# Optimization experiments

Measured on AMD Instinct MI355X. Metric: run time of the kernel, lower is better.

## Reference

```python
import jax, jax.numpy as jnp
import numpy as np

B, N, D, OUT, ED = 8, 256, 128, 128, 1

def setup_inputs() -> dict:
    key = jax.random.key(0)
    ks = jax.random.split(key, 10)
    in2 = 2 * D + ED  # 257
    s = lambda f: 1.0 / np.sqrt(f)
    return {
        "h": jax.random.normal(ks[0], (B, N, D), dtype=jnp.float32),
        "adj": jax.random.randint(ks[1], (B, N, N), 0, 2, dtype=jnp.int32),
        "dist_matrix": jax.random.uniform(ks[2], (B, N, N), dtype=jnp.float32),
        "Wm1": jax.random.uniform(ks[3], (in2, OUT), minval=-s(in2), maxval=s(in2)),
        "bm1": jnp.zeros((OUT,), jnp.float32),
        "Wm2": jax.random.uniform(ks[4], (OUT, OUT), minval=-s(OUT), maxval=s(OUT)),
        "bm2": jnp.zeros((OUT,), jnp.float32),
        "Wa": jax.random.uniform(ks[5], (in2, 1), minval=-s(in2), maxval=s(in2)),
        "ba": jnp.zeros((1,), jnp.float32),
        "Wu": jax.random.uniform(ks[6], (D + OUT, OUT), minval=-s(D + OUT), maxval=s(D + OUT)),
        "bu": jnp.zeros((OUT,), jnp.float32),
    }

def reference(h, adj, dist_matrix, Wm1, bm1, Wm2, bm2, Wa, ba, Wu, bu):
    # h: (B,N,D); adj,dist: (B,N,N)
    Bb, Nn, Dd = h.shape
    h_i = jnp.broadcast_to(h[:, :, None, :], (Bb, Nn, Nn, Dd))
    h_j = jnp.broadcast_to(h[:, None, :, :], (Bb, Nn, Nn, Dd))
    d_ij = dist_matrix[..., None]
    msg_input = jnp.concatenate([h_i, h_j, d_ij], axis=-1)  # (B,N,N,2D+1)
    # message MLP: Linear -> ReLU -> Linear
    msg = jax.nn.relu(msg_input @ Wm1 + bm1) @ Wm2 + bm2    # (B,N,N,OUT)
    # attention MLP: Linear -> LeakyReLU(0.2)
    attn = jax.nn.leaky_relu(msg_input @ Wa + ba, 0.2)      # (B,N,N,1)
    mask = adj[..., None].astype(msg.dtype)                  # (B,N,N,1)
    attn = jnp.where(mask == 0, jnp.asarray(-1e9, attn.dtype), attn)
    attn = jax.nn.softmax(attn, axis=2)                      # softmax over j
    agg = jnp.sum(attn * msg * mask, axis=2)                 # (B,N,OUT)
    h_new = jax.nn.relu(jnp.concatenate([h, agg], axis=-1) @ Wu + bu)
    return h_new
```

## Files before the change

kernel.cpp:

```cpp
#include <hip/hip_runtime.h>

#define BB 8
#define NN 256
#define DD 128
#define OC 128

__global__ __launch_bounds__(128) void precompute_kernel(
    const float* __restrict__ h, const float* __restrict__ Wm1,
    const float* __restrict__ Wa,
    float* __restrict__ preA, float* __restrict__ preB,
    float* __restrict__ ai, float* __restrict__ aj)
{
    const int row = blockIdx.x;
    const int k   = threadIdx.x;

    __shared__ float hrow[DD];
    hrow[k] = h[row * DD + k];
    __syncthreads();

    float accA = 0.f, accB = 0.f;
    #pragma unroll 8
    for (int d = 0; d < DD; ++d) {
        const float hv = hrow[d];
        accA = fmaf(hv, Wm1[d * OC + k], accA);
        accB = fmaf(hv, Wm1[(DD + d) * OC + k], accB);
    }
    preA[row * OC + k] = accA;
    preB[row * OC + k] = accB;

    float vi = hrow[k] * Wa[k];
    float vj = hrow[k] * Wa[DD + k];
    #pragma unroll
    for (int off = 32; off > 0; off >>= 1) {
        vi += __shfl_down(vi, off, 64);
        vj += __shfl_down(vj, off, 64);
    }
    __shared__ float red[4];
    if ((k & 63) == 0) { red[(k >> 6) * 2] = vi; red[(k >> 6) * 2 + 1] = vj; }
    __syncthreads();
    if (k == 0) { ai[row] = red[0] + red[2]; aj[row] = red[1] + red[3]; }
}

__global__ __launch_bounds__(256) void gnn_main_kernel(
    const float* __restrict__ h, const int* __restrict__ adj,
    const float* __restrict__ dist,
    const float* __restrict__ Wm1, const float* __restrict__ bm1,
    const float* __restrict__ Wm2, const float* __restrict__ bm2,
    const float* __restrict__ Wa,  const float* __restrict__ ba,
    const float* __restrict__ Wu,  const float* __restrict__ bu,
    const float* __restrict__ preA, const float* __restrict__ preB,
    const float* __restrict__ aiArr, const float* __restrict__ ajArr,
    float* __restrict__ out)
{
    const int row  = blockIdx.x;
    const int b    = row >> 8;
    const int tid  = threadIdx.x;
    const int k    = tid & (OC - 1);
    const int half = tid >> 7;

    __shared__ float w_sh[NN];
    __shared__ float d_sh[NN];
    __shared__ float red_sh[256];
    __shared__ float t_sh[OC];
    __shared__ float agg_sh[OC];
    __shared__ float preA_sh[OC];
    __shared__ float hrow_sh[DD];
    __shared__ float wsum_sh;

    const int   j  = tid;
    const float dv = dist[row * NN + j];
    const int   mk = adj[row * NN + j];
    d_sh[j] = dv;

    float logit = aiArr[row] + ajArr[b * NN + j] + dv * Wa[2 * DD] + ba[0];
    logit = (logit >= 0.f) ? logit : 0.2f * logit;
    if (mk == 0) logit = -1e9f;

    red_sh[tid] = logit;
    __syncthreads();
    #pragma unroll
    for (int s = 128; s > 0; s >>= 1) {
        if (tid < s) red_sh[tid] = fmaxf(red_sh[tid], red_sh[tid + s]);
        __syncthreads();
    }
    const float mx = red_sh[0];
    __syncthreads();

    const float e = __expf(logit - mx);
    red_sh[tid] = e;
    __syncthreads();
    #pragma unroll
    for (int s = 128; s > 0; s >>= 1) {
        if (tid < s) red_sh[tid] += red_sh[tid + s];
        __syncthreads();
    }
    const float esum = red_sh[0];
    const float w = mk ? (e / esum) : 0.f;
    w_sh[j] = w;
    __syncthreads();

    red_sh[tid] = w;
    if (tid < OC)   preA_sh[tid]        = preA[row * OC + tid];
    if (tid >= 128) hrow_sh[tid - 128]  = h[row * DD + (tid - 128)];
    __syncthreads();
    #pragma unroll
    for (int s = 128; s > 0; s >>= 1) {
        if (tid < s) red_sh[tid] += red_sh[tid + s];
        __syncthreads();
    }
    if (tid == 0) wsum_sh = red_sh[0];
    __syncthreads();

    const float wm1d = Wm1[2 * DD * OC + k];
    const float bm1k = bm1[k];
    const float pa   = preA_sh[k];
    const float* __restrict__ pB = preB + b * NN * OC;

    float acc = 0.f;
    const int j0 = half * 128;
    for (int jj = j0; jj < j0 + 128; ++jj) {
        const float wj = w_sh[jj];
        if (wj != 0.f) {
            float val = fmaf(d_sh[jj], wm1d, pa + pB[jj * OC + k]) + bm1k;
            acc = fmaf(wj, fmaxf(val, 0.f), acc);
        }
    }
    red_sh[tid] = acc;
    __syncthreads();
    if (tid < OC) t_sh[tid] = red_sh[tid] + red_sh[tid + 128];
    __syncthreads();

    float aggacc = 0.f;
    const int m0 = half * 64;
    #pragma unroll 4
    for (int m = m0; m < m0 + 64; ++m)
        aggacc = fmaf(t_sh[m], Wm2[m * OC + k], aggacc);
    red_sh[tid] = aggacc;
    __syncthreads();
    if (tid < OC) agg_sh[tid] = red_sh[tid] + red_sh[tid + 128] + bm2[tid] * wsum_sh;
    __syncthreads();

    float outacc = 0.f;
    if (half == 0) {
        #pragma unroll 4
        for (int d2 = 0; d2 < DD; ++d2)
            outacc = fmaf(hrow_sh[d2], Wu[d2 * OC + k], outacc);
    } else {
        #pragma unroll 4
        for (int m = 0; m < OC; ++m)
            outacc = fmaf(agg_sh[m], Wu[(DD + m) * OC + k], outacc);
    }
    red_sh[tid] = outacc;
    __syncthreads();
    if (tid < OC)
        out[row * OC + tid] = fmaxf(red_sh[tid] + red_sh[tid + 128] + bu[tid], 0.f);
}

extern "C" void kernel_launch(void* const* d_in, const int* in_sizes, int n_in,
                              void* d_out, int out_size, void* d_ws, size_t ws_size,
                              hipStream_t stream) {
    const float* h    = (const float*)d_in[0];
    const int*   adj  = (const int*)  d_in[1];
    const float* dist = (const float*)d_in[2];
    const float* Wm1  = (const float*)d_in[3];
    const float* bm1  = (const float*)d_in[4];
    const float* Wm2  = (const float*)d_in[5];
    const float* bm2  = (const float*)d_in[6];
    const float* Wa   = (const float*)d_in[7];
    const float* ba   = (const float*)d_in[8];
    const float* Wu   = (const float*)d_in[9];
    const float* bu   = (const float*)d_in[10];
    float* out = (float*)d_out;

    float* preA = (float*)d_ws;
    float* preB = preA + BB * NN * OC;
    float* ai   = preB + BB * NN * OC;
    float* aj   = ai + BB * NN;

    precompute_kernel<<<BB * NN, 128, 0, stream>>>(h, Wm1, Wa, preA, preB, ai, aj);
    gnn_main_kernel<<<BB * NN, 256, 0, stream>>>(h, adj, dist,
                                                 Wm1, bm1, Wm2, bm2, Wa, ba, Wu, bu,
                                                 preA, preB, ai, aj, out);
}
```

Measured before the change: 125.8 us.

## Split GNN into three kernels with tiled GEMMs and compacted neighbor loop

Replaces the two-kernel design with three kernels. A multi-row precompute GEMM now also produces the h·Wu term. The main kernel uses wave-shuffle softmax reductions and ballot-compacts the active neighbors into shared memory, then loops only over them with float2 loads. A separate batched kernel does the Wm2 and Wu GEMMs over 8 rows with tiled shared weights. The aim is to cut the per-row redundant weight reads and the barrier-heavy tree reductions, at the cost of an extra launch and an intermediate matrix in global memory.

```diff
diff --git a/kernel.cpp b/kernel.cpp
--- a/kernel.cpp
+++ b/kernel.cpp
@@ -1,159 +1,234 @@
 #include <hip/hip_runtime.h>
 
-#define BB 8
 #define NN 256
 #define DD 128
 #define OC 128
 
-__global__ __launch_bounds__(128) void precompute_kernel(
+__global__ __launch_bounds__(256) void k1_pre(
     const float* __restrict__ h, const float* __restrict__ Wm1,
-    const float* __restrict__ Wa,
-    float* __restrict__ preA, float* __restrict__ preB,
-    float* __restrict__ ai, float* __restrict__ aj)
+    const float* __restrict__ Wa, const float* __restrict__ bm1,
+    const float* __restrict__ Wu, const float* __restrict__ ba,
+    float* __restrict__ pre, float* __restrict__ aiv, float* __restrict__ ajv)
 {
-    const int row = blockIdx.x;
-    const int k   = threadIdx.x;
-
-    __shared__ float hrow[DD];
-    hrow[k] = h[row * DD + k];
-    __syncthreads();
-
-    float accA = 0.f, accB = 0.f;
-    #pragma unroll 8
-    for (int d = 0; d < DD; ++d) {
-        const float hv = hrow[d];
-        accA = fmaf(hv, Wm1[d * OC + k], accA);
-        accB = fmaf(hv, Wm1[(DD + d) * OC + k], accB);
-    }
-    preA[row * OC + k] = accA;
-    preB[row * OC + k] = accB;
-
-    float vi = hrow[k] * Wa[k];
-    float vj = hrow[k] * Wa[DD + k];
-    #pragma unroll
-    for (int off = 32; off > 0; off >>= 1) {
-        vi += __shfl_down(vi, off, 64);
-        vj += __shfl_down(vj, off, 64);
-    }
-    __shared__ float red[4];
-    if ((k & 63) == 0) { red[(k >> 6) * 2] = vi; red[(k >> 6) * 2 + 1] = vj; }
-    __syncthreads();
-    if (k == 0) { ai[row] = red[0] + red[2]; aj[row] = red[1] + red[3]; }
-}
-
-__global__ __launch_bounds__(256) void gnn_main_kernel(
-    const float* __restrict__ h, const int* __restrict__ adj,
-    const float* __restrict__ dist,
-    const float* __restrict__ Wm1, const float* __restrict__ bm1,
-    const float* __restrict__ Wm2, const float* __restrict__ bm2,
-    const float* __restrict__ Wa,  const float* __restrict__ ba,
-    const float* __restrict__ Wu,  const float* __restrict__ bu,
-    const float* __restrict__ preA, const float* __restrict__ preB,
-    const float* __restrict__ aiArr, const float* __restrict__ ajArr,
-    float* __restrict__ out)
+    const int tid  = threadIdx.x;
+    const int row0 = blockIdx.x * 4;
+    const int r    = tid >> 6;
+    const int g    = tid & 63;
+
+    __shared__ float h_sh[4][128];
+    __shared__ float w_sh[16][384];
+
+    const float2* h2    = (const float2*)h;
+    const float2* Wm1_2 = (const float2*)Wm1;
+    const float2* Wu_2  = (const float2*)Wu;
+    const float2* Wa2   = (const float2*)Wa;
+
+    ((float2*)h_sh)[tid] = h2[row0 * 64 + tid];
+    __syncthreads();
+
+    {
+        float2 hv = ((const float2*)h_sh[r])[g];
+        float2 wt = Wa2[g], wb = Wa2[64 + g];
+        float vi = hv.x * wt.x + hv.y * wt.y;
+        float vj = hv.x * wb.x + hv.y * wb.y;
+        #pragma unroll
+        for (int o = 1; o < 64; o <<= 1) {
+            vi += __shfl_xor(vi, o, 64);
+            vj += __shfl_xor(vj, o, 64);
+        }
+        if (g == 0) { aiv[row0 + r] = vi + ba[0]; ajv[row0 + r] = vj; }
+    }
+
+    float2 a0{0.f,0.f}, a1{0.f,0.f}, a2{0.f,0.f};
+    for (int c = 0; c < 8; ++c) {
+        const int d0 = c * 16;
+        __syncthreads();
+        #pragma unroll
+        for (int v = 0; v < 12; ++v) {
+            int idx = tid + 256 * v;
+            int dd = idx / 192, cc = idx % 192;
+            int srow = d0 + dd;
+            float2 val;
+            if (cc < 64)       val = Wm1_2[srow * 64 + cc];
+            else if (cc < 128) val = Wm1_2[(128 + srow) * 64 + (cc - 64)];
+            else               val = Wu_2[srow * 64 + (cc - 128)];
+            ((float2*)w_sh[dd])[cc] = val;
+        }
+        __syncthreads();
+        #pragma unroll
+        for (int dd = 0; dd < 16; ++dd) {
+            const float hb = h_sh[r][d0 + dd];
+            const float2* wr2 = (const float2*)w_sh[dd];
+            float2 w0 = wr2[g], w1 = wr2[64 + g], w2v = wr2[128 + g];
+            a0.x = fmaf(hb, w0.x,  a0.x); a0.y = fmaf(hb, w0.y,  a0.y);
+            a1.x = fmaf(hb, w1.x,  a1.x); a1.y = fmaf(hb, w1.y,  a1.y);
+            a2.x = fmaf(hb, w2v.x, a2.x); a2.y = fmaf(hb, w2v.y, a2.y);
+        }
+    }
+    const float2 bb = ((const float2*)bm1)[g];
+    a0.x += bb.x; a0.y += bb.y;
+    float2* pre2 = (float2*)pre;
+    const int rbase = (row0 + r) * 192;
+    pre2[rbase + g]       = a0;
+    pre2[rbase + 64 + g]  = a1;
+    pre2[rbase + 128 + g] = a2;
+}
+
+__global__ __launch_bounds__(256) void k2_main(
+    const int* __restrict__ adj, const float* __restrict__ dist,
+    const float* __restrict__ Wm1, const float* __restrict__ Wa,
+    const float* __restrict__ pre,
+    const float* __restrict__ aiv, const float* __restrict__ ajv,
+    float* __restrict__ tmat, float* __restrict__ sflag)
 {
     const int row  = blockIdx.x;
     const int b    = row >> 8;
     const int tid  = threadIdx.x;
-    const int k    = tid & (OC - 1);
-    const int half = tid >> 7;
-
-    __shared__ float w_sh[NN];
-    __shared__ float d_sh[NN];
-    __shared__ float red_sh[256];
-    __shared__ float t_sh[OC];
-    __shared__ float agg_sh[OC];
-    __shared__ float preA_sh[OC];
-    __shared__ float hrow_sh[DD];
-    __shared__ float wsum_sh;
+    const int lane = tid & 63;
+    const int wid  = tid >> 6;
+
+    __shared__ float4 cwd[4][64];
+    __shared__ float  mx_sh[4], sm_sh[4];
+    __shared__ float2 tred[4][64];
 
     const int   j  = tid;
     const float dv = dist[row * NN + j];
     const int   mk = adj[row * NN + j];
-    d_sh[j] = dv;
-
-    float logit = aiArr[row] + ajArr[b * NN + j] + dv * Wa[2 * DD] + ba[0];
+
+    float logit = aiv[row] + ajv[b * NN + j] + dv * Wa[2 * DD];
     logit = (logit >= 0.f) ? logit : 0.2f * logit;
-    if (mk == 0) logit = -1e9f;
-
-    red_sh[tid] = logit;
-    __syncthreads();
+    const float lmask = mk ? logit : -1e9f;
+
+    float m = lmask;
     #pragma unroll
-    for (int s = 128; s > 0; s >>= 1) {
-        if (tid < s) red_sh[tid] = fmaxf(red_sh[tid], red_sh[tid + s]);
-        __syncthreads();
-    }
-    const float mx = red_sh[0];
-    __syncthreads();
-
-    const float e = __expf(logit - mx);
-    red_sh[tid] = e;
-    __syncthreads();
+    for (int o = 1; o < 64; o <<= 1) m = fmaxf(m, __shfl_xor(m, o, 64));
+    if (lane == 0) mx_sh[wid] = m;
+    __syncthreads();
+    const float mx = fmaxf(fmaxf(mx_sh[0], mx_sh[1]), fmaxf(mx_sh[2], mx_sh[3]));
+
+    float em = mk ? __expf(logit - mx) : 0.f;
+    float s = em;
     #pragma unroll
-    for (int s = 128; s > 0; s >>= 1) {
-        if (tid < s) red_sh[tid] += red_sh[tid + s];
-        __syncthreads();
-    }
-    const float esum = red_sh[0];
-    const float w = mk ? (e / esum) : 0.f;
-    w_sh[j] = w;
-    __syncthreads();
-
-    red_sh[tid] = w;
-    if (tid < OC)   preA_sh[tid]        = preA[row * OC + tid];
-    if (tid >= 128) hrow_sh[tid - 128]  = h[row * DD + (tid - 128)];
-    __syncthreads();
-    #pragma unroll
-    for (int s = 128; s > 0; s >>= 1) {
-        if (tid < s) red_sh[tid] += red_sh[tid + s];
-        __syncthreads();
-    }
-    if (tid == 0) wsum_sh = red_sh[0];
-    __syncthreads();
-
-    const float wm1d = Wm1[2 * DD * OC + k];
-    const float bm1k = bm1[k];
-    const float pa   = preA_sh[k];
-    const float* __restrict__ pB = preB + b * NN * OC;
-
-    float acc = 0.f;
-    const int j0 = half * 128;
-    for (int jj = j0; jj < j0 + 128; ++jj) {
-        const float wj = w_sh[jj];
-        if (wj != 0.f) {
-            float val = fmaf(d_sh[jj], wm1d, pa + pB[jj * OC + k]) + bm1k;
-            acc = fmaf(wj, fmaxf(val, 0.f), acc);
-        }
-    }
-    red_sh[tid] = acc;
-    __syncthreads();
-    if (tid < OC) t_sh[tid] = red_sh[tid] + red_sh[tid + 128];
-    __syncthreads();
-
-    float aggacc = 0.f;
-    const int m0 = half * 64;
-    #pragma unroll 4
-    for (int m = m0; m < m0 + 64; ++m)
-        aggacc = fmaf(t_sh[m], Wm2[m * OC + k], aggacc);
-    red_sh[tid] = aggacc;
-    __syncthreads();
-    if (tid < OC) agg_sh[tid] = red_sh[tid] + red_sh[tid + 128] + bm2[tid] * wsum_sh;
-    __syncthreads();
-
-    float outacc = 0.f;
-    if (half == 0) {
-        #pragma unroll 4
-        for (int d2 = 0; d2 < DD; ++d2)
-            outacc = fmaf(hrow_sh[d2], Wu[d2 * OC + k], outacc);
-    } else {
-        #pragma unroll 4
-        for (int m = 0; m < OC; ++m)
-            outacc = fmaf(agg_sh[m], Wu[(DD + m) * OC + k], outacc);
-    }
-    red_sh[tid] = outacc;
-    __syncthreads();
-    if (tid < OC)
-        out[row * OC + tid] = fmaxf(red_sh[tid] + red_sh[tid + 128] + bu[tid], 0.f);
+    for (int o = 1; o < 64; o <<= 1) s += __shfl_xor(s, o, 64);
+    if (lane == 0) sm_sh[wid] = s;
+    __syncthreads();
+    const float esum = sm_sh[0] + sm_sh[1] + sm_sh[2] + sm_sh[3];
+    const float inv  = (esum > 0.f) ? (1.0f / esum) : 0.f;
+    const float w    = em * inv;
+
+    const unsigned long long act = __ballot(w != 0.f);
+    const int pos = __popcll(act & ((1ull << lane) - 1ull));
+    const int cnt = __popcll(act);
+    if (w != 0.f)
+        cwd[wid][pos] = make_float4(w, dv, __int_as_float(j * 192), 0.f);
+    __syncthreads();
+
+    const float2* pre2 = (const float2*)pre;
+    const float2  pa   = pre2[row * 192 + lane];
+    const float2  wd1  = ((const float2*)Wm1)[(2 * DD * OC) / 2 + lane];
+    const float2* pB   = pre2 + (size_t)b * NN * 192 + 64;
+
+    float2 acc{0.f, 0.f};
+    for (int i = 0; i < cnt; ++i) {
+        float4 c = cwd[wid][i];
+        int off = __float_as_int(c.z);
+        float2 pb = pB[off + lane];
+        float vx = fmaf(c.y, wd1.x, pa.x + pb.x);
+        float vy = fmaf(c.y, wd1.y, pa.y + pb.y);
+        acc.x = fmaf(c.x, fmaxf(vx, 0.f), acc.x);
+        acc.y = fmaf(c.x, fmaxf(vy, 0.f), acc.y);
+    }
+    tred[wid][lane] = acc;
+    __syncthreads();
+    if (tid < 64) {
+        float2 t0 = tred[0][tid], t1 = tred[1][tid];
+        float2 t2v = tred[2][tid], t3 = tred[3][tid];
+        float2 tt{t0.x + t1.x + t2v.x + t3.x, t0.y + t1.y + t2v.y + t3.y};
+        ((float2*)tmat)[row * 64 + tid] = tt;
+    }
+    if (tid == 0) sflag[row] = (esum > 0.f) ? 1.f : 0.f;
+}
+
+__global__ __launch_bounds__(256) void k3_out(
+    const float* __restrict__ tmat, const float* __restrict__ sflag,
+    const float* __restrict__ pre,
+    const float* __restrict__ Wm2, const float* __restrict__ bm2,
+    const float* __restrict__ Wu,  const float* __restrict__ bu,
+    float* __restrict__ out)
+{
+    const int tid  = threadIdx.x;
+    const int row0 = blockIdx.x * 8;
+    const int r    = tid >> 5;
+    const int g    = tid & 31;
+
+    __shared__ float t_sh[8][128];
+    __shared__ float agg_sh[8][128];
+    __shared__ float w_sh[16][128];
+    __shared__ float sf_sh[8];
+
+    const float2* t2 = (const float2*)tmat;
+    ((float2*)t_sh)[tid]       = t2[row0 * 64 + tid];
+    ((float2*)t_sh)[tid + 256] = t2[row0 * 64 + tid + 256];
+    if (tid < 8) sf_sh[tid] = sflag[row0 + tid];
+
+    const float2* Wm2_2 = (const float2*)Wm2;
+    const float2* Wu_2  = (const float2*)Wu;
+
+    float2 a0{0.f,0.f}, a1{0.f,0.f};
+    for (int c = 0; c < 8; ++c) {
+        const int d0 = c * 16;
+        __syncthreads();
+        #pragma unroll
+        for (int v = 0; v < 4; ++v) {
+            int idx = tid + 256 * v;
+            int dd = idx >> 6, cc = idx & 63;
+            ((float2*)w_sh)[idx] = Wm2_2[(d0 + dd) * 64 + cc];
+        }
+        __syncthreads();
+        #pragma unroll
+        for (int dd = 0; dd < 16; ++dd) {
+            const float tb = t_sh[r][d0 + dd];
+            const float2* wr2 = (const float2*)w_sh[dd];
+            float2 w0 = wr2[g], w1 = wr2[32 + g];
+            a0.x = fmaf(tb, w0.x, a0.x); a0.y = fmaf(tb, w0.y, a0.y);
+            a1.x = fmaf(tb, w1.x, a1.x); a1.y = fmaf(tb, w1.y, a1.y);
+        }
+    }
+    const float sf = sf_sh[r];
+    const float2 b0 = ((const float2*)bm2)[g], b1 = ((const float2*)bm2)[32 + g];
+    ((float2*)agg_sh[r])[g]      = make_float2(fmaf(b0.x, sf, a0.x), fmaf(b0.y, sf, a0.y));
+    ((float2*)agg_sh[r])[32 + g] = make_float2(fmaf(b1.x, sf, a1.x), fmaf(b1.y, sf, a1.y));
+
+    a0 = make_float2(0.f, 0.f); a1 = make_float2(0.f, 0.f);
+    for (int c = 0; c < 8; ++c) {
+        const int d0 = c * 16;
+        __syncthreads();
+        #pragma unroll
+        for (int v = 0; v < 4; ++v) {
+            int idx = tid + 256 * v;
+            int dd = idx >> 6, cc = idx & 63;
+            ((float2*)w_sh)[idx] = Wu_2[(128 + d0 + dd) * 64 + cc];
+        }
+        __syncthreads();
+        #pragma unroll
+        for (int dd = 0; dd < 16; ++dd) {
+            const float ab = agg_sh[r][d0 + dd];
+            const float2* wr2 = (const float2*)w_sh[dd];
+            float2 w0 = wr2[g], w1 = wr2[32 + g];
+            a0.x = fmaf(ab, w0.x, a0.x); a0.y = fmaf(ab, w0.y, a0.y);
+            a1.x = fmaf(ab, w1.x, a1.x); a1.y = fmaf(ab, w1.y, a1.y);
+        }
+    }
+
+    const float2* pre2 = (const float2*)pre;
+    const int prow = (row0 + r) * 192 + 128;
+    float2 hu0 = pre2[prow + g], hu1 = pre2[prow + 32 + g];
+    float2 c0 = ((const float2*)bu)[g], c1 = ((const float2*)bu)[32 + g];
+    float2 o0{fmaxf(a0.x + hu0.x + c0.x, 0.f), fmaxf(a0.y + hu0.y + c0.y, 0.f)};
+    float2 o1{fmaxf(a1.x + hu1.x + c1.x, 0.f), fmaxf(a1.y + hu1.y + c1.y, 0.f)};
+    float2* out2 = (float2*)out;
+    out2[(row0 + r) * 64 + g]      = o0;
+    out2[(row0 + r) * 64 + 32 + g] = o1;
 }
 
 extern "C" void kernel_launch(void* const* d_in, const int* in_sizes, int n_in,
@@ -172,13 +247,13 @@
     const float* bu   = (const float*)d_in[10];
     float* out = (float*)d_out;
 
-    float* preA = (float*)d_ws;
-    float* preB = preA + BB * NN * OC;
-    float* ai   = preB + BB * NN * OC;
-    float* aj   = ai + BB * NN;
-
-    precompute_kernel<<<BB * NN, 128, 0, stream>>>(h, Wm1, Wa, preA, preB, ai, aj);
-    gnn_main_kernel<<<BB * NN, 256, 0, stream>>>(h, adj, dist,
-                                                 Wm1, bm1, Wm2, bm2, Wa, ba, Wu, bu,
-                                                 preA, preB, ai, aj, out);
-}
+    float* pre   = (float*)d_ws;
+    float* aiv   = pre + 2048 * 384;
+    float* ajv   = aiv + 2048;
+    float* tmat  = ajv + 2048;
+    float* sfl   = tmat + 2048 * 128;
+
+    k1_pre <<<512, 256, 0, stream>>>(h, Wm1, Wa, bm1, Wu, ba, pre, aiv, ajv);
+    k2_main<<<2048, 256, 0, stream>>>(adj, dist, Wm1, Wa, pre, aiv, ajv, tmat, sfl);
+    k3_out <<<256, 256, 0, stream>>>(tmat, sfl, pre, Wm2, bm2, Wu, bu, out);
+}
```

Result: slower. 133.6 us (+6.2%).

## Split GNN into three wave-per-row kernels with compacted neighbor lists

Applied to the files above, without the earlier changes.

Replaces the two-kernel design with three kernels that each map one 64-lane wave to a row. The precompute kernel now also folds in the h·Wu half of the update and the bm1 bias, using readlane broadcasts and float2 loads. The main kernel does the softmax with wave shuffles instead of shared-memory tree reductions, compacts the non-zero neighbours via ballot/popcount, and loops only over those. The Wm2 and Wu matmuls move into a separate output kernel. This cuts barriers and predicated loop iterations, at the cost of an extra launch and a round trip of intermediate results through global memory.

```diff
diff --git a/kernel.cpp b/kernel.cpp
--- a/kernel.cpp
+++ b/kernel.cpp
@@ -1,159 +1,215 @@
 #include <hip/hip_runtime.h>
 
-#define BB 8
 #define NN 256
 #define DD 128
 #define OC 128
 
-__global__ __launch_bounds__(128) void precompute_kernel(
+__device__ __forceinline__ float bcastf(float x, int lane) {
+    return __int_as_float(__builtin_amdgcn_readlane(__float_as_int(x), lane));
+}
+
+__global__ __launch_bounds__(256) void k1_pre(
     const float* __restrict__ h, const float* __restrict__ Wm1,
-    const float* __restrict__ Wa,
-    float* __restrict__ preA, float* __restrict__ preB,
-    float* __restrict__ ai, float* __restrict__ aj)
+    const float* __restrict__ Wa, const float* __restrict__ bm1,
+    const float* __restrict__ Wu, const float* __restrict__ ba,
+    float* __restrict__ pre, float* __restrict__ aiv, float* __restrict__ ajv)
 {
-    const int row = blockIdx.x;
-    const int k   = threadIdx.x;
-
-    __shared__ float hrow[DD];
-    hrow[k] = h[row * DD + k];
-    __syncthreads();
-
-    float accA = 0.f, accB = 0.f;
-    #pragma unroll 8
-    for (int d = 0; d < DD; ++d) {
-        const float hv = hrow[d];
-        accA = fmaf(hv, Wm1[d * OC + k], accA);
-        accB = fmaf(hv, Wm1[(DD + d) * OC + k], accB);
-    }
-    preA[row * OC + k] = accA;
-    preB[row * OC + k] = accB;
-
-    float vi = hrow[k] * Wa[k];
-    float vj = hrow[k] * Wa[DD + k];
+    const int tid = threadIdx.x;
+    const int l   = tid & 63;
+    const int w   = tid >> 6;
+    const int row = blockIdx.x * 4 + w;
+
+    const float2* h2v   = (const float2*)h;
+    const float2* Wm1_2 = (const float2*)Wm1;
+    const float2* Wu_2  = (const float2*)Wu;
+    const float2* Wa2   = (const float2*)Wa;
+
+    const float2 hl = h2v[row * 64 + l];
+
+    {
+        const float2 wt = Wa2[l], wb = Wa2[64 + l];
+        float vi = hl.x * wt.x + hl.y * wt.y;
+        float vj = hl.x * wb.x + hl.y * wb.y;
+        #pragma unroll
+        for (int o = 1; o < 64; o <<= 1) {
+            vi += __shfl_xor(vi, o, 64);
+            vj += __shfl_xor(vj, o, 64);
+        }
+        if (l == 0) { aiv[row] = vi + ba[0]; ajv[row] = vj; }
+    }
+
+    float2 c0{0.f,0.f}, c1{0.f,0.f}, c2{0.f,0.f};
+    #pragma unroll 4
+    for (int m = 0; m < 64; ++m) {
+        const float hx = bcastf(hl.x, m);
+        const float hy = bcastf(hl.y, m);
+        const int d0 = 2 * m, d1 = 2 * m + 1;
+        const float2 a00 = Wm1_2[d0 * 64 + l],        a01 = Wm1_2[d1 * 64 + l];
+        const float2 b00 = Wm1_2[(DD + d0) * 64 + l], b01 = Wm1_2[(DD + d1) * 64 + l];
+        const float2 u00 = Wu_2[d0 * 64 + l],         u01 = Wu_2[d1 * 64 + l];
+        c0.x = fmaf(hx, a00.x, fmaf(hy, a01.x, c0.x));
+        c0.y = fmaf(hx, a00.y, fmaf(hy, a01.y, c0.y));
+        c1.x = fmaf(hx, b00.x, fmaf(hy, b01.x, c1.x));
+        c1.y = fmaf(hx, b00.y, fmaf(hy, b01.y, c1.y));
+        c2.x = fmaf(hx, u00.x, fmaf(hy, u01.x, c2.x));
+        c2.y = fmaf(hx, u00.y, fmaf(hy, u01.y, c2.y));
+    }
+    const float2 bb = ((const float2*)bm1)[l];
+    c0.x += bb.x; c0.y += bb.y;
+
+    float2* pre2 = (float2*)pre;
+    const int rb = row * 192;
+    pre2[rb + l]       = c0;
+    pre2[rb + 64 + l]  = c1;
+    pre2[rb + 128 + l] = c2;
+}
+
+__global__ __launch_bounds__(256) void k2_main(
+    const int* __restrict__ adj, const float* __restrict__ dist,
+    const float* __restrict__ Wm1, const float* __restrict__ Wa,
+    const float* __restrict__ pre,
+    const float* __restrict__ aiv, const float* __restrict__ ajv,
+    float* __restrict__ tmat, float* __restrict__ sflag)
+{
+    const int tid  = threadIdx.x;
+    const int l    = tid & 63;
+    const int wid  = tid >> 6;
+    const int r    = wid >> 1;
+    const int half = wid & 1;
+    const int row  = blockIdx.x * 2 + r;
+    const int b    = row >> 8;
+
+    __shared__ float  mx_sh[4], sm_sh[4];
+    __shared__ float4 cw[4][128];
+    __shared__ float2 accb[2][64];
+
+    const int   jb  = half * 128;
+    const int2  mk2 = ((const int2*)  (adj  + row * NN))[half * 64 + l];
+    const float2 dv2 = ((const float2*)(dist + row * NN))[half * 64 + l];
+    const float2 aj2 = ((const float2*)(ajv  + b   * NN))[half * 64 + l];
+    const float ai = aiv[row];
+    const float dc = Wa[2 * DD];
+
+    float l0 = ai + aj2.x + dv2.x * dc;
+    float l1 = ai + aj2.y + dv2.y * dc;
+    l0 = (l0 >= 0.f) ? l0 : 0.2f * l0;
+    l1 = (l1 >= 0.f) ? l1 : 0.2f * l1;
+    const float l0m = mk2.x ? l0 : -1e9f;
+    const float l1m = mk2.y ? l1 : -1e9f;
+
+    float m = fmaxf(l0m, l1m);
     #pragma unroll
-    for (int off = 32; off > 0; off >>= 1) {
-        vi += __shfl_down(vi, off, 64);
-        vj += __shfl_down(vj, off, 64);
-    }
-    __shared__ float red[4];
-    if ((k & 63) == 0) { red[(k >> 6) * 2] = vi; red[(k >> 6) * 2 + 1] = vj; }
-    __syncthreads();
-    if (k == 0) { ai[row] = red[0] + red[2]; aj[row] = red[1] + red[3]; }
-}
-
-__global__ __launch_bounds__(256) void gnn_main_kernel(
-    const float* __restrict__ h, const int* __restrict__ adj,
-    const float* __restrict__ dist,
-    const float* __restrict__ Wm1, const float* __restrict__ bm1,
+    for (int o = 1; o < 64; o <<= 1) m = fmaxf(m, __shfl_xor(m, o, 64));
+    if (l == 0) mx_sh[wid] = m;
+    __syncthreads();
+    const float mx = fmaxf(mx_sh[r * 2], mx_sh[r * 2 + 1]);
+
+    const float e0 = mk2.x ? __expf(l0 - mx) : 0.f;
+    const float e1 = mk2.y ? __expf(l1 - mx) : 0.f;
+    float s = e0 + e1;
+    #pragma unroll
+    for (int o = 1; o < 64; o <<= 1) s += __shfl_xor(s, o, 64);
+    if (l == 0) sm_sh[wid] = s;
+    __syncthreads();
+    const float esum = sm_sh[r * 2] + sm_sh[r * 2 + 1];
+    const float inv  = (esum > 0.f) ? (1.0f / esum) : 0.f;
+    const float w0 = e0 * inv, w1 = e1 * inv;
+
+    const unsigned long long below = (1ull << l) - 1ull;
+    const unsigned long long m0 = __ballot(w0 != 0.f);
+    const unsigned long long m1 = __ballot(w1 != 0.f);
+    const int c0n = __popcll(m0);
+    const int cnt = c0n + __popcll(m1);
+    const int j0 = jb + 2 * l;
+    if (w0 != 0.f)
+        cw[wid][__popcll(m0 & below)]       = make_float4(w0, dv2.x, __int_as_float(j0 * 192), 0.f);
+    if (w1 != 0.f)
+        cw[wid][c0n + __popcll(m1 & below)] = make_float4(w1, dv2.y, __int_as_float((j0 + 1) * 192), 0.f);
+    __syncthreads();
+    const float4 g0 = cw[wid][l];
+    const float4 g1 = cw[wid][64 + l];
+
+    const float2* pre2 = (const float2*)pre;
+    const float2  pa   = pre2[row * 192 + l];
+    const float2  wd1  = ((const float2*)Wm1)[(2 * DD * OC) / 2 + l];
+    const float2* pBb  = pre2 + (size_t)b * NN * 192 + 64;
+
+    float2 acc{0.f, 0.f};
+    const int n0 = cnt < 64 ? cnt : 64;
+    for (int p = 0; p < n0; ++p) {
+        const float wp  = bcastf(g0.x, p);
+        const float dp  = bcastf(g0.y, p);
+        const int   jof = __builtin_amdgcn_readlane(__float_as_int(g0.z), p);
+        const float2 pb = pBb[jof + l];
+        const float vx = fmaf(dp, wd1.x, pa.x + pb.x);
+        const float vy = fmaf(dp, wd1.y, pa.y + pb.y);
+        acc.x = fmaf(wp, fmaxf(vx, 0.f), acc.x);
+        acc.y = fmaf(wp, fmaxf(vy, 0.f), acc.y);
+    }
+    for (int p = 64; p < cnt; ++p) {
+        const float wp  = bcastf(g1.x, p - 64);
+        const float dp  = bcastf(g1.y, p - 64);
+        const int   jof = __builtin_amdgcn_readlane(__float_as_int(g1.z), p - 64);
+        const float2 pb = pBb[jof + l];
+        const float vx = fmaf(dp, wd1.x, pa.x + pb.x);
+        const float vy = fmaf(dp, wd1.y, pa.y + pb.y);
+        acc.x = fmaf(wp, fmaxf(vx, 0.f), acc.x);
+        acc.y = fmaf(wp, fmaxf(vy, 0.f), acc.y);
+    }
+
+    if (half == 1) accb[r][l] = acc;
+    __syncthreads();
+    if (half == 0) {
+        const float2 o = accb[r][l];
+        float2 t{acc.x + o.x, acc.y + o.y};
+        ((float2*)tmat)[row * 64 + l] = t;
+        if (l == 0) sflag[row] = (esum > 0.f) ? 1.f : 0.f;
+    }
+}
+
+__global__ __launch_bounds__(256) void k3_out(
+    const float* __restrict__ tmat, const float* __restrict__ sflag,
+    const float* __restrict__ pre,
     const float* __restrict__ Wm2, const float* __restrict__ bm2,
-    const float* __restrict__ Wa,  const float* __restrict__ ba,
     const float* __restrict__ Wu,  const float* __restrict__ bu,
-    const float* __restrict__ preA, const float* __restrict__ preB,
-    const float* __restrict__ aiArr, const float* __restrict__ ajArr,
     float* __restrict__ out)
 {
-    const int row  = blockIdx.x;
-    const int b    = row >> 8;
-    const int tid  = threadIdx.x;
-    const int k    = tid & (OC - 1);
-    const int half = tid >> 7;
-
-    __shared__ float w_sh[NN];
-    __shared__ float d_sh[NN];
-    __shared__ float red_sh[256];
-    __shared__ float t_sh[OC];
-    __shared__ float agg_sh[OC];
-    __shared__ float preA_sh[OC];
-    __shared__ float hrow_sh[DD];
-    __shared__ float wsum_sh;
-
-    const int   j  = tid;
-    const float dv = dist[row * NN + j];
-    const int   mk = adj[row * NN + j];
-    d_sh[j] = dv;
-
-    float logit = aiArr[row] + ajArr[b * NN + j] + dv * Wa[2 * DD] + ba[0];
-    logit = (logit >= 0.f) ? logit : 0.2f * logit;
-    if (mk == 0) logit = -1e9f;
-
-    red_sh[tid] = logit;
-    __syncthreads();
-    #pragma unroll
-    for (int s = 128; s > 0; s >>= 1) {
-        if (tid < s) red_sh[tid] = fmaxf(red_sh[tid], red_sh[tid + s]);
-        __syncthreads();
-    }
-    const float mx = red_sh[0];
-    __syncthreads();
-
-    const float e = __expf(logit - mx);
-    red_sh[tid] = e;
-    __syncthreads();
-    #pragma unroll
-    for (int s = 128; s > 0; s >>= 1) {
-        if (tid < s) red_sh[tid] += red_sh[tid + s];
-        __syncthreads();
-    }
-    const float esum = red_sh[0];
-    const float w = mk ? (e / esum) : 0.f;
-    w_sh[j] = w;
-    __syncthreads();
-
-    red_sh[tid] = w;
-    if (tid < OC)   preA_sh[tid]        = preA[row * OC + tid];
-    if (tid >= 128) hrow_sh[tid - 128]  = h[row * DD + (tid - 128)];
-    __syncthreads();
-    #pragma unroll
-    for (int s = 128; s > 0; s >>= 1) {
-        if (tid < s) red_sh[tid] += red_sh[tid + s];
-        __syncthreads();
-    }
-    if (tid == 0) wsum_sh = red_sh[0];
-    __syncthreads();
-
-    const float wm1d = Wm1[2 * DD * OC + k];
-    const float bm1k = bm1[k];
-    const float pa   = preA_sh[k];
-    const float* __restrict__ pB = preB + b * NN * OC;
-
-    float acc = 0.f;
-    const int j0 = half * 128;
-    for (int jj = j0; jj < j0 + 128; ++jj) {
-        const float wj = w_sh[jj];
-        if (wj != 0.f) {
-            float val = fmaf(d_sh[jj], wm1d, pa + pB[jj * OC + k]) + bm1k;
-            acc = fmaf(wj, fmaxf(val, 0.f), acc);
-        }
-    }
-    red_sh[tid] = acc;
-    __syncthreads();
-    if (tid < OC) t_sh[tid] = red_sh[tid] + red_sh[tid + 128];
-    __syncthreads();
-
-    float aggacc = 0.f;
-    const int m0 = half * 64;
+    const int tid = threadIdx.x;
+    const int l   = tid & 63;
+    const int w   = tid >> 6;
+    const int row = blockIdx.x * 4 + w;
+
+    const float2* Wm2_2 = (const float2*)Wm2;
+    const float2* Wu_2  = (const float2*)Wu;
+    const float2 t2 = ((const float2*)tmat)[row * 64 + l];
+    const float  sf = sflag[row];
+
+    float2 a{0.f, 0.f};
     #pragma unroll 4
-    for (int m = m0; m < m0 + 64; ++m)
-        aggacc = fmaf(t_sh[m], Wm2[m * OC + k], aggacc);
-    red_sh[tid] = aggacc;
-    __syncthreads();
-    if (tid < OC) agg_sh[tid] = red_sh[tid] + red_sh[tid + 128] + bm2[tid] * wsum_sh;
-    __syncthreads();
-
-    float outacc = 0.f;
-    if (half == 0) {
-        #pragma unroll 4
-        for (int d2 = 0; d2 < DD; ++d2)
-            outacc = fmaf(hrow_sh[d2], Wu[d2 * OC + k], outacc);
-    } else {
-        #pragma unroll 4
-        for (int m = 0; m < OC; ++m)
-            outacc = fmaf(agg_sh[m], Wu[(DD + m) * OC + k], outacc);
-    }
-    red_sh[tid] = outacc;
-    __syncthreads();
-    if (tid < OC)
-        out[row * OC + tid] = fmaxf(red_sh[tid] + red_sh[tid + 128] + bu[tid], 0.f);
+    for (int m = 0; m < 64; ++m) {
+        const float tx = bcastf(t2.x, m);
+        const float ty = bcastf(t2.y, m);
+        const float2 q0 = Wm2_2[(2 * m) * 64 + l], q1 = Wm2_2[(2 * m + 1) * 64 + l];
+        a.x = fmaf(tx, q0.x, fmaf(ty, q1.x, a.x));
+        a.y = fmaf(tx, q0.y, fmaf(ty, q1.y, a.y));
+    }
+    const float2 b2 = ((const float2*)bm2)[l];
+    a.x = fmaf(b2.x, sf, a.x);
+    a.y = fmaf(b2.y, sf, a.y);
+
+    float2 o{0.f, 0.f};
+    #pragma unroll 4
+    for (int m = 0; m < 64; ++m) {
+        const float ax = bcastf(a.x, m);
+        const float ay = bcastf(a.y, m);
+        const float2 q0 = Wu_2[(DD + 2 * m) * 64 + l], q1 = Wu_2[(DD + 2 * m + 1) * 64 + l];
+        o.x = fmaf(ax, q0.x, fmaf(ay, q1.x, o.x));
+        o.y = fmaf(ax, q0.y, fmaf(ay, q1.y, o.y));
+    }
+    const float2 hu = ((const float2*)pre)[row * 192 + 128 + l];
+    const float2 bl = ((const float2*)bu)[l];
+    float2 res{fmaxf(o.x + hu.x + bl.x, 0.f), fmaxf(o.y + hu.y + bl.y, 0.f)};
+    ((float2*)out)[row * 64 + l] = res;
 }
 
 extern "C" void kernel_launch(void* const* d_in, const int* in_sizes, int n_in,
@@ -172,13 +228,13 @@
     const float* bu   = (const float*)d_in[10];
     float* out = (float*)d_out;
 
-    float* preA = (float*)d_ws;
-    float* preB = preA + BB * NN * OC;
-    float* ai   = preB + BB * NN * OC;
-    float* aj   = ai + BB * NN;
-
-    precompute_kernel<<<BB * NN, 128, 0, stream>>>(h, Wm1, Wa, preA, preB, ai, aj);
-    gnn_main_kernel<<<BB * NN, 256, 0, stream>>>(h, adj, dist,
-                                                 Wm1, bm1, Wm2, bm2, Wa, ba, Wu, bu,
-                                                 preA, preB, ai, aj, out);
-}
+    float* pre  = (float*)d_ws;
+    float* aiv  = pre + 2048 * 384;
+    float* ajv  = aiv + 2048;
+    float* tmat = ajv + 2048;
+    float* sfl  = tmat + 2048 * 128;
+
+    k1_pre <<<512,  256, 0, stream>>>(h, Wm1, Wa, bm1, Wu, ba, pre, aiv, ajv);
+    k2_main<<<1024, 256, 0, stream>>>(adj, dist, Wm1, Wa, pre, aiv, ajv, tmat, sfl);
+    k3_out <<<512,  256, 0, stream>>>(tmat, sfl, pre, Wm2, bm2, Wu, bu, out);
+}
```

Measured after the change: 136.8 us. 8.7% more time.

## Restructure both kernels to process four rows per block with wave-level reductions

Applied to the files above, without the earlier changes.

Both kernels now handle four rows per 256-thread block, one wavefront per row. The main kernel does the masked softmax with in-wave xor shuffles instead of shared-memory tree reductions and many barriers, and broadcasts weights with readlane. The precompute kernel also computes the h·Wu half of the update projection and folds bm1 and ba into the precomputed values, stored in an interleaved 384-wide buffer read with float2/float4 loads. The intent is to cut synchronisation overhead and reuse the Wm2/Wu weight loads across four rows, at the cost of fewer blocks (512) and a serial 256-step gather per wave.

```diff
diff --git a/kernel.cpp b/kernel.cpp
--- a/kernel.cpp
+++ b/kernel.cpp
@@ -1,159 +1,211 @@
 #include <hip/hip_runtime.h>
 
-#define BB 8
 #define NN 256
 #define DD 128
 #define OC 128
 
-__global__ __launch_bounds__(128) void precompute_kernel(
+__device__ __forceinline__ float bcastf(float x, int lane) {
+    return __int_as_float(__builtin_amdgcn_readlane(__float_as_int(x), lane));
+}
+
+__global__ __launch_bounds__(256) void k1_pre(
     const float* __restrict__ h, const float* __restrict__ Wm1,
-    const float* __restrict__ Wa,
-    float* __restrict__ preA, float* __restrict__ preB,
-    float* __restrict__ ai, float* __restrict__ aj)
+    const float* __restrict__ Wa, const float* __restrict__ bm1,
+    const float* __restrict__ Wu, const float* __restrict__ ba,
+    float* __restrict__ pre, float* __restrict__ aiv, float* __restrict__ ajv)
 {
-    const int row = blockIdx.x;
-    const int k   = threadIdx.x;
-
-    __shared__ float hrow[DD];
-    hrow[k] = h[row * DD + k];
-    __syncthreads();
-
-    float accA = 0.f, accB = 0.f;
-    #pragma unroll 8
-    for (int d = 0; d < DD; ++d) {
-        const float hv = hrow[d];
-        accA = fmaf(hv, Wm1[d * OC + k], accA);
-        accB = fmaf(hv, Wm1[(DD + d) * OC + k], accB);
-    }
-    preA[row * OC + k] = accA;
-    preB[row * OC + k] = accB;
-
-    float vi = hrow[k] * Wa[k];
-    float vj = hrow[k] * Wa[DD + k];
-    #pragma unroll
-    for (int off = 32; off > 0; off >>= 1) {
-        vi += __shfl_down(vi, off, 64);
-        vj += __shfl_down(vj, off, 64);
-    }
-    __shared__ float red[4];
-    if ((k & 63) == 0) { red[(k >> 6) * 2] = vi; red[(k >> 6) * 2 + 1] = vj; }
-    __syncthreads();
-    if (k == 0) { ai[row] = red[0] + red[2]; aj[row] = red[1] + red[3]; }
-}
-
-__global__ __launch_bounds__(256) void gnn_main_kernel(
-    const float* __restrict__ h, const int* __restrict__ adj,
-    const float* __restrict__ dist,
-    const float* __restrict__ Wm1, const float* __restrict__ bm1,
+    const int tid  = threadIdx.x;
+    const int l    = tid & 63;
+    const int w    = tid >> 6;
+    const int row0 = blockIdx.x * 4;
+
+    const float2* h2 = (const float2*)h;
+    float2 hr[4];
+    #pragma unroll
+    for (int r = 0; r < 4; ++r) hr[r] = h2[(row0 + r) * 64 + l];
+
+    if (w == 3) {
+        const float2* Wa2 = (const float2*)Wa;
+        const float2 wt = Wa2[l], wb = Wa2[64 + l];
+        float vi[4], vj[4];
+        #pragma unroll
+        for (int r = 0; r < 4; ++r) {
+            vi[r] = hr[r].x * wt.x + hr[r].y * wt.y;
+            vj[r] = hr[r].x * wb.x + hr[r].y * wb.y;
+        }
+        #pragma unroll
+        for (int o = 1; o < 64; o <<= 1) {
+            #pragma unroll
+            for (int r = 0; r < 4; ++r) {
+                vi[r] += __shfl_xor(vi[r], o, 64);
+                vj[r] += __shfl_xor(vj[r], o, 64);
+            }
+        }
+        if (l == 0) {
+            const float b0 = ba[0];
+            #pragma unroll
+            for (int r = 0; r < 4; ++r) {
+                aiv[row0 + r] = vi[r] + b0;
+                ajv[row0 + r] = vj[r];
+            }
+        }
+        return;
+    }
+
+    const float2* W2 = (w == 0) ? (const float2*)Wm1
+                     : (w == 1) ? (const float2*)Wm1 + DD * 64
+                                : (const float2*)Wu;
+
+    float2 acc[4];
+    #pragma unroll
+    for (int r = 0; r < 4; ++r) acc[r] = make_float2(0.f, 0.f);
+
+    #pragma unroll 4
+    for (int m = 0; m < 64; ++m) {
+        const float2 w0 = W2[(2 * m) * 64 + l];
+        const float2 w1 = W2[(2 * m + 1) * 64 + l];
+        #pragma unroll
+        for (int r = 0; r < 4; ++r) {
+            const float hx = bcastf(hr[r].x, m);
+            const float hy = bcastf(hr[r].y, m);
+            acc[r].x = fmaf(hx, w0.x, fmaf(hy, w1.x, acc[r].x));
+            acc[r].y = fmaf(hx, w0.y, fmaf(hy, w1.y, acc[r].y));
+        }
+    }
+    if (w == 0) {
+        const float2 bb = ((const float2*)bm1)[l];
+        #pragma unroll
+        for (int r = 0; r < 4; ++r) { acc[r].x += bb.x; acc[r].y += bb.y; }
+    }
+    float2* pre2 = (float2*)pre;
+    #pragma unroll
+    for (int r = 0; r < 4; ++r)
+        pre2[(row0 + r) * 192 + w * 64 + l] = acc[r];
+}
+
+__global__ __launch_bounds__(256) void k2_main(
+    const int* __restrict__ adj, const float* __restrict__ dist,
+    const float* __restrict__ Wm1, const float* __restrict__ Wa,
+    const float* __restrict__ pre,
+    const float* __restrict__ aiv, const float* __restrict__ ajv,
     const float* __restrict__ Wm2, const float* __restrict__ bm2,
-    const float* __restrict__ Wa,  const float* __restrict__ ba,
     const float* __restrict__ Wu,  const float* __restrict__ bu,
-    const float* __restrict__ preA, const float* __restrict__ preB,
-    const float* __restrict__ aiArr, const float* __restrict__ ajArr,
     float* __restrict__ out)
 {
-    const int row  = blockIdx.x;
+    const int tid  = threadIdx.x;
+    const int l    = tid & 63;
+    const int w    = tid >> 6;
+    const int row0 = blockIdx.x * 4;
+    const int row  = row0 + w;
     const int b    = row >> 8;
-    const int tid  = threadIdx.x;
-    const int k    = tid & (OC - 1);
-    const int half = tid >> 7;
-
-    __shared__ float w_sh[NN];
-    __shared__ float d_sh[NN];
-    __shared__ float red_sh[256];
-    __shared__ float t_sh[OC];
-    __shared__ float agg_sh[OC];
-    __shared__ float preA_sh[OC];
-    __shared__ float hrow_sh[DD];
-    __shared__ float wsum_sh;
-
-    const int   j  = tid;
-    const float dv = dist[row * NN + j];
-    const int   mk = adj[row * NN + j];
-    d_sh[j] = dv;
-
-    float logit = aiArr[row] + ajArr[b * NN + j] + dv * Wa[2 * DD] + ba[0];
-    logit = (logit >= 0.f) ? logit : 0.2f * logit;
-    if (mk == 0) logit = -1e9f;
-
-    red_sh[tid] = logit;
+
+    __shared__ float t_sh[4][128];
+    __shared__ float agg_sh[4][128];
+    __shared__ float sf_sh[4];
+
+    const int4   mk4 = ((const int4*)  (adj  + row * NN))[l];
+    const float4 dv4 = ((const float4*)(dist + row * NN))[l];
+    const float4 aj4 = ((const float4*)(ajv  + b   * NN))[l];
+    const float  ai  = aiv[row];
+    const float  dc  = Wa[2 * DD];
+
+    float lg[4];
+    lg[0] = ai + aj4.x + dv4.x * dc;
+    lg[1] = ai + aj4.y + dv4.y * dc;
+    lg[2] = ai + aj4.z + dv4.z * dc;
+    lg[3] = ai + aj4.w + dv4.w * dc;
+    #pragma unroll
+    for (int c = 0; c < 4; ++c) lg[c] = (lg[c] >= 0.f) ? lg[c] : 0.2f * lg[c];
+    const int mk[4] = {mk4.x, mk4.y, mk4.z, mk4.w};
+
+    float m = -1e9f;
+    #pragma unroll
+    for (int c = 0; c < 4; ++c) if (mk[c]) m = fmaxf(m, lg[c]);
+    #pragma unroll
+    for (int o = 1; o < 64; o <<= 1) m = fmaxf(m, __shfl_xor(m, o, 64));
+
+    float e[4], s = 0.f;
+    #pragma unroll
+    for (int c = 0; c < 4; ++c) { e[c] = mk[c] ? __expf(lg[c] - m) : 0.f; s += e[c]; }
+    #pragma unroll
+    for (int o = 1; o < 64; o <<= 1) s += __shfl_xor(s, o, 64);
+    const float inv = (s > 0.f) ? (1.0f / s) : 0.f;
+    float wj0 = e[0] * inv, wj1 = e[1] * inv, wj2 = e[2] * inv, wj3 = e[3] * inv;
+
+    const float2* pre2 = (const float2*)pre;
+    const float2  pa   = pre2[row * 192 + l];
+    const float2  wd1  = ((const float2*)Wm1)[2 * DD * 64 + l];
+    const float2* pBb  = pre2 + (size_t)b * NN * 192 + 64;
+
+    float2 acc = make_float2(0.f, 0.f);
+    for (int p = 0; p < 64; ++p) {
+        const float sw0 = bcastf(wj0, p), sd0 = bcastf(dv4.x, p);
+        const float sw1 = bcastf(wj1, p), sd1 = bcastf(dv4.y, p);
+        const float sw2 = bcastf(wj2, p), sd2 = bcastf(dv4.z, p);
+        const float sw3 = bcastf(wj3, p), sd3 = bcastf(dv4.w, p);
+        const int jb = 4 * p;
+        if (sw0 != 0.f) {
+            const float2 pb = pBb[jb * 192 + l];
+            const float vx = fmaf(sd0, wd1.x, pa.x + pb.x);
+            const float vy = fmaf(sd0, wd1.y, pa.y + pb.y);
+            acc.x = fmaf(sw0, fmaxf(vx, 0.f), acc.x);
+            acc.y = fmaf(sw0, fmaxf(vy, 0.f), acc.y);
+        }
+        if (sw1 != 0.f) {
+            const float2 pb = pBb[(jb + 1) * 192 + l];
+            const float vx = fmaf(sd1, wd1.x, pa.x + pb.x);
+            const float vy = fmaf(sd1, wd1.y, pa.y + pb.y);
+            acc.x = fmaf(sw1, fmaxf(vx, 0.f), acc.x);
+            acc.y = fmaf(sw1, fmaxf(vy, 0.f), acc.y);
+        }
+        if (sw2 != 0.f) {
+            const float2 pb = pBb[(jb + 2) * 192 + l];
+            const float vx = fmaf(sd2, wd1.x, pa.x + pb.x);
+            const float vy = fmaf(sd2, wd1.y, pa.y + pb.y);
+            acc.x = fmaf(sw2, fmaxf(vx, 0.f), acc.x);
+            acc.y = fmaf(sw2, fmaxf(vy, 0.f), acc.y);
+        }
+        if (sw3 != 0.f) {
+            const float2 pb = pBb[(jb + 3) * 192 + l];
+            const float vx = fmaf(sd3, wd1.x, pa.x + pb.x);
+            const float vy = fmaf(sd3, wd1.y, pa.y + pb.y);
+            acc.x = fmaf(sw3, fmaxf(vx, 0.f), acc.x);
+            acc.y = fmaf(sw3, fmaxf(vy, 0.f), acc.y);
+        }
+    }
+    t_sh[w][2 * l]     = acc.x;
+    t_sh[w][2 * l + 1] = acc.y;
+    if (l == 0) sf_sh[w] = (s > 0.f) ? 1.f : 0.f;
     __syncthreads();
-    #pragma unroll
-    for (int s = 128; s > 0; s >>= 1) {
-        if (tid < s) red_sh[tid] = fmaxf(red_sh[tid], red_sh[tid + s]);
-        __syncthreads();
-    }
-    const float mx = red_sh[0];
+
+    const int c   = 32 * w + (l & 31);
+    const int rsl = l >> 5;
+    float a[2];
+    #pragma unroll
+    for (int pass = 0; pass < 2; ++pass) {
+        const int r = 2 * pass + rsl;
+        float av = 0.f;
+        #pragma unroll 8
+        for (int k = 0; k < 128; ++k)
+            av = fmaf(t_sh[r][k], Wm2[k * OC + c], av);
+        a[pass] = fmaf(bm2[c], sf_sh[r], av);
+    }
+    #pragma unroll
+    for (int pass = 0; pass < 2; ++pass)
+        agg_sh[2 * pass + rsl][c] = a[pass];
     __syncthreads();
 
-    const float e = __expf(logit - mx);
-    red_sh[tid] = e;
-    __syncthreads();
-    #pragma unroll
-    for (int s = 128; s > 0; s >>= 1) {
-        if (tid < s) red_sh[tid] += red_sh[tid + s];
-        __syncthreads();
-    }
-    const float esum = red_sh[0];
-    const float w = mk ? (e / esum) : 0.f;
-    w_sh[j] = w;
-    __syncthreads();
-
-    red_sh[tid] = w;
-    if (tid < OC)   preA_sh[tid]        = preA[row * OC + tid];
-    if (tid >= 128) hrow_sh[tid - 128]  = h[row * DD + (tid - 128)];
-    __syncthreads();
-    #pragma unroll
-    for (int s = 128; s > 0; s >>= 1) {
-        if (tid < s) red_sh[tid] += red_sh[tid + s];
-        __syncthreads();
-    }
-    if (tid == 0) wsum_sh = red_sh[0];
-    __syncthreads();
-
-    const float wm1d = Wm1[2 * DD * OC + k];
-    const float bm1k = bm1[k];
-    const float pa   = preA_sh[k];
-    const float* __restrict__ pB = preB + b * NN * OC;
-
-    float acc = 0.f;
-    const int j0 = half * 128;
-    for (int jj = j0; jj < j0 + 128; ++jj) {
-        const float wj = w_sh[jj];
-        if (wj != 0.f) {
-            float val = fmaf(d_sh[jj], wm1d, pa + pB[jj * OC + k]) + bm1k;
-            acc = fmaf(wj, fmaxf(val, 0.f), acc);
-        }
-    }
-    red_sh[tid] = acc;
-    __syncthreads();
-    if (tid < OC) t_sh[tid] = red_sh[tid] + red_sh[tid + 128];
-    __syncthreads();
-
-    float aggacc = 0.f;
-    const int m0 = half * 64;
-    #pragma unroll 4
-    for (int m = m0; m < m0 + 64; ++m)
-        aggacc = fmaf(t_sh[m], Wm2[m * OC + k], aggacc);
-    red_sh[tid] = aggacc;
-    __syncthreads();
-    if (tid < OC) agg_sh[tid] = red_sh[tid] + red_sh[tid + 128] + bm2[tid] * wsum_sh;
-    __syncthreads();
-
-    float outacc = 0.f;
-    if (half == 0) {
-        #pragma unroll 4
-        for (int d2 = 0; d2 < DD; ++d2)
-            outacc = fmaf(hrow_sh[d2], Wu[d2 * OC + k], outacc);
-    } else {
-        #pragma unroll 4
-        for (int m = 0; m < OC; ++m)
-            outacc = fmaf(agg_sh[m], Wu[(DD + m) * OC + k], outacc);
-    }
-    red_sh[tid] = outacc;
-    __syncthreads();
-    if (tid < OC)
-        out[row * OC + tid] = fmaxf(red_sh[tid] + red_sh[tid + 128] + bu[tid], 0.f);
+    const float buc = bu[c];
+    #pragma unroll
+    for (int pass = 0; pass < 2; ++pass) {
+        const int r = 2 * pass + rsl;
+        float ov = 0.f;
+        #pragma unroll 8
+        for (int k = 0; k < 128; ++k)
+            ov = fmaf(agg_sh[r][k], Wu[(DD + k) * OC + c], ov);
+        const float hu = pre[(row0 + r) * 384 + 256 + c];
+        out[(row0 + r) * OC + c] = fmaxf(ov + hu + buc, 0.f);
+    }
 }
 
 extern "C" void kernel_launch(void* const* d_in, const int* in_sizes, int n_in,
@@ -172,13 +224,11 @@
     const float* bu   = (const float*)d_in[10];
     float* out = (float*)d_out;
 
-    float* preA = (float*)d_ws;
-    float* preB = preA + BB * NN * OC;
-    float* ai   = preB + BB * NN * OC;
-    float* aj   = ai + BB * NN;
-
-    precompute_kernel<<<BB * NN, 128, 0, stream>>>(h, Wm1, Wa, preA, preB, ai, aj);
-    gnn_main_kernel<<<BB * NN, 256, 0, stream>>>(h, adj, dist,
-                                                 Wm1, bm1, Wm2, bm2, Wa, ba, Wu, bu,
-                                                 preA, preB, ai, aj, out);
-}
+    float* pre = (float*)d_ws;
+    float* aiv = pre + 2048 * 384;
+    float* ajv = aiv + 2048;
+
+    k1_pre <<<512, 256, 0, stream>>>(h, Wm1, Wa, bm1, Wu, ba, pre, aiv, ajv);
+    k2_main<<<512, 256, 0, stream>>>(adj, dist, Wm1, Wa, pre, aiv, ajv,
+                                     Wm2, bm2, Wu, bu, out);
+}
```

New measurement: 132.2 us. +5.0%, slower.
